# Kernel tuning notes

Hardware: AMD Instinct MI355X
Metric: run time of the kernel (lower is better)

The kernel has to match this reference:

```python
import jax, jax.numpy as jnp
import numpy as np

B, T, C, H = 8, 2048, 1024, 128  # batch, seq (=block_size), n_embd, head_size


def setup_inputs() -> dict:
    key = jax.random.key(0)
    kx, kk, kq, kv = jax.random.split(key, 4)
    x = jax.random.normal(kx, (B, T, C), dtype=jnp.float32)
    # nn.Linear(n_embd, head_size, bias=False) weights, stored as (in, out) for x @ W
    s = 1.0 / np.sqrt(C)
    Wk = jax.random.normal(kk, (C, H), dtype=jnp.float32) * s
    Wq = jax.random.normal(kq, (C, H), dtype=jnp.float32) * s
    Wv = jax.random.normal(kv, (C, H), dtype=jnp.float32) * s
    return {"x": x, "Wk": Wk, "Wq": Wq, "Wv": Wv}


def reference(x, Wk, Wq, Wv):
    # x: [B, T, C]
    Bx, Tx, Cx = x.shape
    k = x @ Wk  # [B, T, H]
    q = x @ Wq  # [B, T, H]
    v = x @ Wv  # [B, T, H]
    # NOTE: source multiplies by C**0.5 (not 1/sqrt), kept faithfully
    wei = jnp.einsum("bth,bsh->bts", q, k) * (Cx ** 0.5)  # [B, T, T]
    causal = jnp.tril(jnp.ones((Tx, Tx), dtype=bool))
    wei = jnp.where(causal, wei, -jnp.inf)
    wei = jax.nn.softmax(wei, axis=-1)
    # dropout omitted (eval-mode reference)
    return wei @ v  # [B, T, H]
```

## Files before the change

kernel.cpp:

```cpp
#include <hip/hip_runtime.h>

constexpr int kB = 8;
constexpr int kT = 2048;
constexpr int kC = 1024;
constexpr int kH = 128;
constexpr int kM = kB * kT;
constexpr size_t kMH = (size_t)kM * kH;
constexpr size_t kWH = (size_t)kC * kH;

#define QSCALE 46.166241308446828f

typedef __attribute__((ext_vector_type(8))) short bf16x8;
typedef __attribute__((ext_vector_type(4))) float f32x4;


__device__ inline unsigned short f2bf_rne(float f) {
    union { float f; unsigned int u; } x; x.f = f;
    unsigned int r = x.u + 0x7fff + ((x.u >> 16) & 1);
    return (unsigned short)(r >> 16);
}
__device__ inline float bf2f(unsigned short h) {
    union { float f; unsigned int u; } x; x.u = ((unsigned int)h) << 16;
    return x.f;
}
__device__ inline unsigned int pack_hi2(float a, float b) {
    return __builtin_amdgcn_perm(__float_as_uint(b), __float_as_uint(a),
                                 0x07060302u);
}
__device__ inline float hi_part(float v) {
    return __uint_as_float(__float_as_uint(v) & 0xffff0000u);
}
__device__ inline void load_lds16(const unsigned short* g, unsigned short* l) {
    __builtin_amdgcn_global_load_lds(
        (const __attribute__((address_space(1))) unsigned int*)g,
        (__attribute__((address_space(3))) unsigned int*)l, 16, 0, 0);
}
__device__ inline float fexp2(float x) { return __builtin_amdgcn_exp2f(x); }

template <int CTRL>
__device__ inline float dpp_rot(float x) {
    return __int_as_float(__builtin_amdgcn_update_dpp(
        0, __float_as_int(x), CTRL, 0xf, 0xf, false));
}
__device__ inline float rowmax16(float x) {
    x = fmaxf(x, dpp_rot<0x121>(x));
    x = fmaxf(x, dpp_rot<0x122>(x));
    x = fmaxf(x, dpp_rot<0x124>(x));
    x = fmaxf(x, dpp_rot<0x128>(x));
    return x;
}
__device__ inline float rowsum16(float x) {
    x += dpp_rot<0x121>(x);
    x += dpp_rot<0x122>(x);
    x += dpp_rot<0x124>(x);
    x += dpp_rot<0x128>(x);
    return x;
}

__global__ __launch_bounds__(256) void prep_w(
    const float* __restrict__ Wk, const float* __restrict__ Wq,
    const float* __restrict__ Wv, unsigned short* __restrict__ ws)
{
    const int h = blockIdx.x;
    const int mat = blockIdx.y;
    const float* W = (mat == 0) ? Wq : (mat == 1) ? Wk : Wv;
    unsigned short* hi = ws + 5 * kMH + (size_t)(mat * 2) * kWH;
    unsigned short* lo = hi + kWH;

    const int k0 = threadIdx.x * 4;
    unsigned short hv[4], lv[4];
#pragma unroll
    for (int j = 0; j < 4; ++j) {
        const float f = W[(size_t)(k0 + j) * kH + h];
        hv[j] = f2bf_rne(f);
        lv[j] = f2bf_rne(f - bf2f(hv[j]));
    }
    *(uint2*)&hi[(size_t)h * kC + k0] =
        make_uint2(((unsigned)hv[1] << 16) | hv[0], ((unsigned)hv[3] << 16) | hv[2]);
    *(uint2*)&lo[(size_t)h * kC + k0] =
        make_uint2(((unsigned)lv[1] << 16) | lv[0], ((unsigned)lv[3] << 16) | lv[2]);
}

__global__ __launch_bounds__(256) void qkv_mfma(
    const float* __restrict__ x, unsigned short* __restrict__ ws)
{
    __shared__ __align__(16) unsigned short Bh[128 * 64];
    __shared__ __align__(16) unsigned short Bl[128 * 64];

    const int idx = blockIdx.x;
    const int mat = idx >> 8;
    const int m0 = (idx & 255) * 64;
    const unsigned short* wThi = ws + 5 * kMH + (size_t)(mat * 2) * kWH;
    const unsigned short* wTlo = wThi + kWH;

    const int tid = threadIdx.x;
    const int w = tid >> 6, lane = tid & 63;
    const int li = lane & 15, quad = lane >> 4;

    const float* xrow = x + (size_t)(m0 + w * 16 + li) * kC;

    f32x4 acc[8];
#pragma unroll
    for (int j = 0; j < 8; ++j) acc[j] = (f32x4){0.f, 0.f, 0.f, 0.f};

    for (int kt = 0; kt < kC; kt += 64) {
        if (kt) __syncthreads();
#pragma unroll
        for (int u = 0; u < 4; ++u) {
            const int f = u * 256 + tid;
            const int row = f >> 3, g = (f & 7) ^ (row & 7);
            load_lds16(wThi + (size_t)row * kC + kt + g * 8, Bh + f * 8);
            if (mat <= 1)
                load_lds16(wTlo + (size_t)row * kC + kt + g * 8, Bl + f * 8);
        }
        float4 xa[2][2];
#pragma unroll
        for (int kc = 0; kc < 2; ++kc) {
            xa[kc][0] = *(const float4*)(xrow + kt + kc * 32 + quad * 8);
            xa[kc][1] = *(const float4*)(xrow + kt + kc * 32 + quad * 8 + 4);
        }
        bf16x8 ah[2], al[2];
        if (mat <= 1) {
#pragma unroll
            for (int kc = 0; kc < 2; ++kc) {
                const float4 a0 = xa[kc][0], a1 = xa[kc][1];
                unsigned int hp[4], lp[4];
                hp[0] = pack_hi2(a0.x, a0.y); hp[1] = pack_hi2(a0.z, a0.w);
                hp[2] = pack_hi2(a1.x, a1.y); hp[3] = pack_hi2(a1.z, a1.w);
                lp[0] = pack_hi2(a0.x - hi_part(a0.x), a0.y - hi_part(a0.y));
                lp[1] = pack_hi2(a0.z - hi_part(a0.z), a0.w - hi_part(a0.w));
                lp[2] = pack_hi2(a1.x - hi_part(a1.x), a1.y - hi_part(a1.y));
                lp[3] = pack_hi2(a1.z - hi_part(a1.z), a1.w - hi_part(a1.w));
                ah[kc] = *(bf16x8*)hp;
                al[kc] = *(bf16x8*)lp;
            }
        } else {
#pragma unroll
            for (int kc = 0; kc < 2; ++kc) {
                const float4 a0 = xa[kc][0], a1 = xa[kc][1];
                unsigned short e[8];
                e[0] = f2bf_rne(a0.x); e[1] = f2bf_rne(a0.y);
                e[2] = f2bf_rne(a0.z); e[3] = f2bf_rne(a0.w);
                e[4] = f2bf_rne(a1.x); e[5] = f2bf_rne(a1.y);
                e[6] = f2bf_rne(a1.z); e[7] = f2bf_rne(a1.w);
                ah[kc] = *(bf16x8*)e;
            }
        }
        __syncthreads();

        if (mat <= 1) {
#pragma unroll
            for (int kc = 0; kc < 2; ++kc)
#pragma unroll
                for (int nt = 0; nt < 8; ++nt) {
                    const int row = nt * 16 + li;
                    const int pos = (kc * 4 + quad) ^ (row & 7);
                    const bf16x8 bh = *(const bf16x8*)&Bh[row * 64 + pos * 8];
                    const bf16x8 bl = *(const bf16x8*)&Bl[row * 64 + pos * 8];
                    acc[nt] = __builtin_amdgcn_mfma_f32_16x16x32_bf16(ah[kc], bh, acc[nt], 0, 0, 0);
                    acc[nt] = __builtin_amdgcn_mfma_f32_16x16x32_bf16(al[kc], bh, acc[nt], 0, 0, 0);
                    acc[nt] = __builtin_amdgcn_mfma_f32_16x16x32_bf16(ah[kc], bl, acc[nt], 0, 0, 0);
                }
        } else {
#pragma unroll
            for (int kc = 0; kc < 2; ++kc)
#pragma unroll
                for (int nt = 0; nt < 8; ++nt) {
                    const int row = nt * 16 + li;
                    const int pos = (kc * 4 + quad) ^ (row & 7);
                    const bf16x8 bh = *(const bf16x8*)&Bh[row * 64 + pos * 8];
                    acc[nt] = __builtin_amdgcn_mfma_f32_16x16x32_bf16(ah[kc], bh, acc[nt], 0, 0, 0);
                }
        }
    }

    if (mat <= 1) {
        unsigned short* hip_ = ws + (size_t)(mat * 2) * kMH;
        unsigned short* lop  = hip_ + kMH;
        const float sc = (mat == 0) ? QSCALE : 1.0f;
#pragma unroll
        for (int nt = 0; nt < 8; ++nt) {
            const int col = nt * 16 + li;
#pragma unroll
            for (int reg = 0; reg < 4; ++reg) {
                const int row = m0 + w * 16 + quad * 4 + reg;
                const float v = acc[nt][reg] * sc;
                hip_[(size_t)row * kH + col] = (unsigned short)(__float_as_uint(v) >> 16);
                lop[(size_t)row * kH + col] =
                    (unsigned short)(__float_as_uint(v - hi_part(v)) >> 16);
            }
        }
    } else {
        unsigned short* vt = ws + 4 * kMH;
        const int bb = m0 >> 11;
        const int t0 = (m0 & (kT - 1)) + w * 16 + quad * 4;
#pragma unroll
        for (int nt = 0; nt < 8; ++nt) {
            const int h = nt * 16 + li;
            ushort4 pk;
            pk.x = f2bf_rne(acc[nt][0]);
            pk.y = f2bf_rne(acc[nt][1]);
            pk.z = f2bf_rne(acc[nt][2]);
            pk.w = f2bf_rne(acc[nt][3]);
            *(ushort4*)&vt[((size_t)(bb * kH + h)) * kT + t0] = pk;
        }
    }
}

__global__ __launch_bounds__(256, 2) void attn_mfma(
    const unsigned short* __restrict__ ws, float* __restrict__ out)
{
    __shared__ __align__(16) unsigned short Ps[4][2][16][40];
    __shared__ __align__(16) float Ml[4][32][2];
    __shared__ __align__(16) float Obuf[3][32][128];

    const int tid = threadIdx.x;
    const int w = tid >> 6, lane = tid & 63;
    const int li = lane & 15, quad = lane >> 4;

    const int idx = blockIdx.x;
    const int b = idx & 7;
    const int j = idx >> 3;
    const int qt = (j < 32) ? j : 95 - j;
    const int i0 = qt * 32;
    const int nc = qt + 1;

    const unsigned short* qhi = ws;
    const unsigned short* qlo = ws + kMH;
    const unsigned short* khi = ws + 2 * kMH;
    const unsigned short* klo = ws + 3 * kMH;
    const unsigned short* vt  = ws + 4 * kMH;

    bf16x8 qh[2][4], ql[2][4];
#pragma unroll
    for (int mi = 0; mi < 2; ++mi) {
        const size_t qoff = ((size_t)(b * kT + i0 + mi * 16 + li)) * kH;
#pragma unroll
        for (int kc = 0; kc < 4; ++kc) {
            qh[mi][kc] = *(const bf16x8*)(qhi + qoff + kc * 32 + quad * 8);
            ql[mi][kc] = *(const bf16x8*)(qlo + qoff + kc * 32 + quad * 8);
        }
    }

    f32x4 o[2][8];
#pragma unroll
    for (int mi = 0; mi < 2; ++mi)
#pragma unroll
        for (int ht = 0; ht < 8; ++ht) o[mi][ht] = (f32x4){0.f, 0.f, 0.f, 0.f};
    float m_i[2][4], l_i[2][4];
#pragma unroll
    for (int mi = 0; mi < 2; ++mi)
#pragma unroll
        for (int reg = 0; reg < 4; ++reg) { m_i[mi][reg] = -3.0e38f; l_i[mi][reg] = 0.f; }

    for (int jc = w; jc < nc; jc += 4) {
        const int t0 = jc * 32;
        bf16x8 vf[8];
#pragma unroll
        for (int ht = 0; ht < 8; ++ht)
            vf[ht] = *(const bf16x8*)(vt + (size_t)(b * kH + ht * 16 + li) * kT +
                                      t0 + quad * 8);
        f32x4 s[2][2];
#pragma unroll
        for (int mi = 0; mi < 2; ++mi)
#pragma unroll
            for (int nt = 0; nt < 2; ++nt) s[mi][nt] = (f32x4){0.f, 0.f, 0.f, 0.f};
        bf16x8 kh[2][2], kl[2][2];
#pragma unroll
        for (int nt = 0; nt < 2; ++nt) {
            const size_t ka =
                ((size_t)(b * kT + t0 + nt * 16 + li)) * kH + quad * 8;
            kh[0][nt] = *(const bf16x8*)(khi + ka);
            kl[0][nt] = *(const bf16x8*)(klo + ka);
        }
#pragma unroll
        for (int kc = 0; kc < 4; ++kc) {
            const int cur = kc & 1, nxt = cur ^ 1;
            if (kc < 3) {
#pragma unroll
                for (int nt = 0; nt < 2; ++nt) {
                    const size_t ka = ((size_t)(b * kT + t0 + nt * 16 + li)) * kH +
                                      (kc + 1) * 32 + quad * 8;
                    kh[nxt][nt] = *(const bf16x8*)(khi + ka);
                    kl[nxt][nt] = *(const bf16x8*)(klo + ka);
                }
            }
#pragma unroll
            for (int mi = 0; mi < 2; ++mi)
#pragma unroll
                for (int nt = 0; nt < 2; ++nt) {
                    s[mi][nt] = __builtin_amdgcn_mfma_f32_16x16x32_bf16(qh[mi][kc], kh[cur][nt], s[mi][nt], 0, 0, 0);
                    s[mi][nt] = __builtin_amdgcn_mfma_f32_16x16x32_bf16(ql[mi][kc], kh[cur][nt], s[mi][nt], 0, 0, 0);
                    s[mi][nt] = __builtin_amdgcn_mfma_f32_16x16x32_bf16(qh[mi][kc], kl[cur][nt], s[mi][nt], 0, 0, 0);
                }
        }
        if (jc == qt) {
#pragma unroll
            for (int mi = 0; mi < 2; ++mi) {
                const int grow0 = i0 + mi * 16 + quad * 4;
#pragma unroll
                for (int nt = 0; nt < 2; ++nt) {
                    const int gcol = t0 + nt * 16 + li;
#pragma unroll
                    for (int reg = 0; reg < 4; ++reg)
                        if (gcol > grow0 + reg) s[mi][nt][reg] = -3.0e38f;
                }
            }
        }
#pragma unroll
        for (int mi = 0; mi < 2; ++mi) {
            float alpha[4];
#pragma unroll
            for (int reg = 0; reg < 4; ++reg) {
                const float mr = rowmax16(fmaxf(s[mi][0][reg], s[mi][1][reg]));
                const float mn = fmaxf(m_i[mi][reg], mr);
                alpha[reg] = fexp2(m_i[mi][reg] - mn);
                m_i[mi][reg] = mn;
                const float p0 = fexp2(s[mi][0][reg] - mn);
                const float p1 = fexp2(s[mi][1][reg] - mn);
                s[mi][0][reg] = p0; s[mi][1][reg] = p1;
                const float rs = rowsum16(p0 + p1);
                l_i[mi][reg] = l_i[mi][reg] * alpha[reg] + rs;
            }
            const f32x4 av = {alpha[0], alpha[1], alpha[2], alpha[3]};
#pragma unroll
            for (int ht = 0; ht < 8; ++ht) o[mi][ht] *= av;
#pragma unroll
            for (int nt = 0; nt < 2; ++nt)
#pragma unroll
                for (int reg = 0; reg < 4; ++reg)
                    Ps[w][mi][quad * 4 + reg][nt * 16 + li] = f2bf_rne(s[mi][nt][reg]);
        }
#pragma unroll
        for (int mi = 0; mi < 2; ++mi) {
            const bf16x8 pf = *(const bf16x8*)&Ps[w][mi][li][quad * 8];
#pragma unroll
            for (int ht = 0; ht < 8; ++ht)
                o[mi][ht] = __builtin_amdgcn_mfma_f32_16x16x32_bf16(pf, vf[ht], o[mi][ht], 0, 0, 0);
        }
    }

    if (li == 0) {
#pragma unroll
        for (int mi = 0; mi < 2; ++mi)
#pragma unroll
            for (int reg = 0; reg < 4; ++reg) {
                Ml[w][mi * 16 + quad * 4 + reg][0] = m_i[mi][reg];
                Ml[w][mi * 16 + quad * 4 + reg][1] = l_i[mi][reg];
            }
    }
    __syncthreads();
    float a_self[2][4], linv[2][4];
#pragma unroll
    for (int mi = 0; mi < 2; ++mi)
#pragma unroll
        for (int reg = 0; reg < 4; ++reg) {
            const int row = mi * 16 + quad * 4 + reg;
            const float m0_ = Ml[0][row][0], m1 = Ml[1][row][0];
            const float m2 = Ml[2][row][0], m3 = Ml[3][row][0];
            const float ms = fmaxf(fmaxf(m0_, m1), fmaxf(m2, m3));
            const float L = Ml[0][row][1] * fexp2(m0_ - ms) +
                            Ml[1][row][1] * fexp2(m1 - ms) +
                            Ml[2][row][1] * fexp2(m2 - ms) +
                            Ml[3][row][1] * fexp2(m3 - ms);
            a_self[mi][reg] = fexp2(m_i[mi][reg] - ms);
            linv[mi][reg] = 1.0f / L;
        }
    if (w) {
#pragma unroll
        for (int mi = 0; mi < 2; ++mi)
#pragma unroll
            for (int ht = 0; ht < 8; ++ht)
#pragma unroll
                for (int reg = 0; reg < 4; ++reg)
                    Obuf[w - 1][mi * 16 + quad * 4 + reg][ht * 16 + li] =
                        o[mi][ht][reg] * a_self[mi][reg];
    }
    __syncthreads();
    if (w == 0) {
#pragma unroll
        for (int mi = 0; mi < 2; ++mi)
#pragma unroll
            for (int ht = 0; ht < 8; ++ht)
#pragma unroll
                for (int reg = 0; reg < 4; ++reg) {
                    const int row = mi * 16 + quad * 4 + reg;
                    const int col = ht * 16 + li;
                    const float v = o[mi][ht][reg] * a_self[mi][reg] +
                                    Obuf[0][row][col] + Obuf[1][row][col] +
                                    Obuf[2][row][col];
                    out[(size_t)(b * kT + i0 + row) * kH + col] = v * linv[mi][reg];
                }
    }
}

extern "C" void kernel_launch(void* const* d_in, const int* in_sizes, int n_in,
                              void* d_out, int out_size, void* d_ws, size_t ws_size,
                              hipStream_t stream) {
    const float* x  = (const float*)d_in[0];
    const float* Wk = (const float*)d_in[1];
    const float* Wq = (const float*)d_in[2];
    const float* Wv = (const float*)d_in[3];
    unsigned short* ws = (unsigned short*)d_ws;
    float* out = (float*)d_out;

    hipLaunchKernelGGL(prep_w, dim3(128, 3), dim3(256), 0, stream, Wk, Wq, Wv, ws);
    hipLaunchKernelGGL(qkv_mfma, dim3(768), dim3(256), 0, stream, x, ws);
    hipLaunchKernelGGL(attn_mfma, dim3(512), dim3(256), 0, stream,
                       (const unsigned short*)ws, out);
}
```

Measured before the change: 187.7 us.

## Split attention KV chunks across eight waves with serialized LDS reduction

Doubles the attention block to 512 threads (8 waves), so each query tile's key chunks are spread over eight waves instead of four. The cross-wave merge now folds each wave's partial output into a single LDS buffer in eight serialized phases, each followed by a barrier, and all waves share the final normalized store. This cuts the per-wave serial chunk loop, which matters for the long causal tiles, and reduces LDS for the output buffer. In exchange it adds eight block barriers, and the launch bound of 4 blocks of 512 threads may squeeze the register budget and cause spills.

After: 331.5 us. 1.77x slower.

```diff
diff --git a/kernel.cpp b/kernel.cpp
--- a/kernel.cpp
+++ b/kernel.cpp
@@ -207,12 +207,12 @@
     }
 }
 
-__global__ __launch_bounds__(256, 2) void attn_mfma(
+__global__ __launch_bounds__(512, 4) void attn_mfma(
     const unsigned short* __restrict__ ws, float* __restrict__ out)
 {
-    __shared__ __align__(16) unsigned short Ps[4][2][16][40];
-    __shared__ __align__(16) float Ml[4][32][2];
-    __shared__ __align__(16) float Obuf[3][32][128];
+    __shared__ __align__(16) unsigned short Ps[8][2][16][40];
+    __shared__ __align__(16) float Ml[8][32][2];
+    __shared__ __align__(16) float Obuf[32][128];
 
     const int tid = threadIdx.x;
     const int w = tid >> 6, lane = tid & 63;
@@ -253,7 +253,7 @@
 #pragma unroll
         for (int reg = 0; reg < 4; ++reg) { m_i[mi][reg] = -3.0e38f; l_i[mi][reg] = 0.f; }
 
-    for (int jc = w; jc < nc; jc += 4) {
+    for (int jc = w; jc < nc; jc += 8) {
         const int t0 = jc * 32;
         bf16x8 vf[8];
 #pragma unroll
@@ -356,41 +356,44 @@
 #pragma unroll
         for (int reg = 0; reg < 4; ++reg) {
             const int row = mi * 16 + quad * 4 + reg;
-            const float m0_ = Ml[0][row][0], m1 = Ml[1][row][0];
-            const float m2 = Ml[2][row][0], m3 = Ml[3][row][0];
-            const float ms = fmaxf(fmaxf(m0_, m1), fmaxf(m2, m3));
-            const float L = Ml[0][row][1] * fexp2(m0_ - ms) +
-                            Ml[1][row][1] * fexp2(m1 - ms) +
-                            Ml[2][row][1] * fexp2(m2 - ms) +
-                            Ml[3][row][1] * fexp2(m3 - ms);
+            float ms = Ml[0][row][0];
+#pragma unroll
+            for (int w2 = 1; w2 < 8; ++w2) ms = fmaxf(ms, Ml[w2][row][0]);
+            float L = 0.f;
+#pragma unroll
+            for (int w2 = 0; w2 < 8; ++w2)
+                L += Ml[w2][row][1] * fexp2(Ml[w2][row][0] - ms);
             a_self[mi][reg] = fexp2(m_i[mi][reg] - ms);
             linv[mi][reg] = 1.0f / L;
         }
-    if (w) {
+#pragma unroll 1
+    for (int ph = 0; ph < 8; ++ph) {
+        if (w == ph) {
+#pragma unroll
+            for (int mi = 0; mi < 2; ++mi)
+#pragma unroll
+                for (int ht = 0; ht < 8; ++ht)
+#pragma unroll
+                    for (int reg = 0; reg < 4; ++reg) {
+                        const int row = mi * 16 + quad * 4 + reg;
+                        const int col = ht * 16 + li;
+                        const float val = o[mi][ht][reg] * a_self[mi][reg];
+                        if (ph == 0) Obuf[row][col] = val;
+                        else         Obuf[row][col] += val;
+                    }
+        }
+        __syncthreads();
+    }
+    {
+        const int col = w * 16 + li;
 #pragma unroll
         for (int mi = 0; mi < 2; ++mi)
 #pragma unroll
-            for (int ht = 0; ht < 8; ++ht)
-#pragma unroll
-                for (int reg = 0; reg < 4; ++reg)
-                    Obuf[w - 1][mi * 16 + quad * 4 + reg][ht * 16 + li] =
-                        o[mi][ht][reg] * a_self[mi][reg];
-    }
-    __syncthreads();
-    if (w == 0) {
-#pragma unroll
-        for (int mi = 0; mi < 2; ++mi)
-#pragma unroll
-            for (int ht = 0; ht < 8; ++ht)
-#pragma unroll
-                for (int reg = 0; reg < 4; ++reg) {
-                    const int row = mi * 16 + quad * 4 + reg;
-                    const int col = ht * 16 + li;
-                    const float v = o[mi][ht][reg] * a_self[mi][reg] +
-                                    Obuf[0][row][col] + Obuf[1][row][col] +
-                                    Obuf[2][row][col];
-                    out[(size_t)(b * kT + i0 + row) * kH + col] = v * linv[mi][reg];
-                }
+            for (int reg = 0; reg < 4; ++reg) {
+                const int row = mi * 16 + quad * 4 + reg;
+                out[(size_t)(b * kT + i0 + row) * kH + col] =
+                    Obuf[row][col] * linv[mi][reg];
+            }
     }
 }
 
@@ -406,6 +409,6 @@
 
     hipLaunchKernelGGL(prep_w, dim3(128, 3), dim3(256), 0, stream, Wk, Wq, Wv, ws);
     hipLaunchKernelGGL(qkv_mfma, dim3(768), dim3(256), 0, stream, x, ws);
-    hipLaunchKernelGGL(attn_mfma, dim3(512), dim3(256), 0, stream,
+    hipLaunchKernelGGL(attn_mfma, dim3(512), dim3(512), 0, stream,
                        (const unsigned short*)ws, out);
 }
```
